# Kernel tuning notes

Measured on AMD Instinct MI355X. Metric: run time of the kernel, lower is better.

## Reference

```python
import jax, jax.numpy as jnp
import numpy as np

RES = 64; UP = 128; LATENT = 16; RGB_LAT = 15
XYZ_MIN = -1.0; XYZ_MAX = 1.0
STEPSIZE = 0.5; NEAR = 0.2; FAR = 6.0; BG = 1.0
VOXEL = (XYZ_MAX - XYZ_MIN) / RES
ALPHA_INIT = 1e-4
ACT_SHIFT = float(np.log(1.0 / (1.0 - ALPHA_INIT) - 1.0))
N_SAMPLES = int(np.linalg.norm(np.array([2 * RES + 1] * 3)) / STEPSIZE) + 1
BN_SCALE = (1.0 + 1e-5) ** -0.5  # eval-mode BatchNorm with running_mean=0, running_var=1
EPS = 1e-12
FREQS = [float(2.0 ** i) for i in range(6)]

def _sobel_kernel():
    hd = np.array([-1., -2., 0., 2., 1.]); h = np.array([1., 4., 6., 4., 1.])
    kx = np.einsum('i,j,k->ijk', hd, h, h)
    ky = np.einsum('i,j,k->ijk', h, hd, h)
    kz = np.einsum('i,j,k->ijk', h, h, hd)
    K = np.stack([kx, ky, kz])[:, None]
    return jnp.asarray(K / np.abs(K).max(), dtype=jnp.float32)

SOBEL_K = _sobel_kernel()

def _normalize(x, axis=-1):
    return x / jnp.maximum(jnp.linalg.norm(x, axis=axis, keepdims=True), EPS)

def _conv1x1(x, w, b):
    return jnp.einsum('oc,cdhw->odhw', w, x) + b[:, None, None, None]

def _bn(x, g, b):
    return x * (BN_SCALE * g)[:, None, None, None] + b[:, None, None, None]

def _prelu(x, a):
    return jnp.where(x >= 0, x, a[:, None, None, None] * x)

def _grid_reg(grid, c1_w, c1_b, bn1_g, bn1_b, pr1_a, c2_w, c2_b, bn2_g, bn2_b, pr2_a, c3_w, c3_b):
    x1 = _prelu(_bn(_conv1x1(grid, c1_w, c1_b), bn1_g, bn1_b), pr1_a)
    x2 = _prelu(_bn(_conv1x1(jnp.concatenate([x1, grid], 0), c2_w, c2_b), bn2_g, bn2_b), pr2_a)
    x3 = _conv1x1(jnp.concatenate([x1, x2, grid], 0), c3_w, c3_b)  # [(1+15)*8, R, R, R]
    # PixelShuffle3d(scale=2): [16*8,R,R,R] -> [16,2R,2R,2R]
    up = x3.reshape(LATENT, 2, 2, 2, RES, RES, RES).transpose(0, 4, 1, 5, 2, 6, 3).reshape(LATENT, UP, UP, UP)
    sob = jax.lax.conv_general_dilated(up[:1][None], SOBEL_K, (1, 1, 1), [(2, 2)] * 3,
                                       dimension_numbers=('NCDHW', 'OIDHW', 'NCDHW'))[0]
    normals = -_normalize(sob, axis=0)
    return up.transpose(1, 2, 3, 0), normals.transpose(1, 2, 3, 0)  # [UP,UP,UP,16], [UP,UP,UP,3]

def _trilinear(feat, p):
    # feat: [UP,UP,UP,C] indexed as world (x,y,z); p: [...,3] world coords. align_corners=True.
    u = jnp.clip((p - XYZ_MIN) / (XYZ_MAX - XYZ_MIN) * (UP - 1), 0.0, UP - 1.0)
    i0 = jnp.clip(jnp.floor(u).astype(jnp.int32), 0, UP - 2)
    f = u - i0.astype(u.dtype)
    ix, iy, iz = i0[..., 0], i0[..., 1], i0[..., 2]
    fx, fy, fz = f[..., 0:1], f[..., 1:2], f[..., 2:3]
    def g(dx, dy, dz):
        return feat[ix + dx, iy + dy, iz + dz]
    c00 = g(0, 0, 0) * (1 - fz) + g(0, 0, 1) * fz
    c01 = g(0, 1, 0) * (1 - fz) + g(0, 1, 1) * fz
    c10 = g(1, 0, 0) * (1 - fz) + g(1, 0, 1) * fz
    c11 = g(1, 1, 0) * (1 - fz) + g(1, 1, 1) * fz
    c0 = c00 * (1 - fy) + c01 * fy
    c1 = c10 * (1 - fy) + c11 * fy
    return c0 * (1 - fx) + c1 * fx

def _sample_ray(rays_o, rays_d):
    vec = jnp.where(rays_d == 0, 1e-6, rays_d)
    rate_a = (XYZ_MAX - rays_o) / vec
    rate_b = (XYZ_MIN - rays_o) / vec
    t_min = jnp.clip(jnp.minimum(rate_a, rate_b).max(-1), NEAR, FAR)
    t_max = jnp.clip(jnp.maximum(rate_a, rate_b).min(-1), NEAR, FAR)
    mask_ray = t_max <= t_min
    rng = jnp.arange(N_SAMPLES, dtype=rays_o.dtype)  # eval mode: no jitter
    step = STEPSIZE * VOXEL * rng
    interpx = t_min[:, None] + step[None] / jnp.linalg.norm(rays_d, axis=-1, keepdims=True)
    pts = rays_o[:, None, :] + rays_d[:, None, :] * interpx[..., None]
    outbox = mask_ray[:, None] | ((pts < XYZ_MIN) | (pts > XYZ_MAX)).any(-1)
    return pts, outbox

def _forward(rays_o, rays_d, viewdirs, grid, c1_w, c1_b, bn1_g, bn1_b, pr1_a, c2_w, c2_b, bn2_g, bn2_b, pr2_a, c3_w, c3_b, mlp_w0, mlp_b0, mlp_w1, mlp_b1, mlp_w2, mlp_b2, mlp_w3, mlp_b3):
    feat_grid, normals_grid = _grid_reg(grid, c1_w, c1_b, bn1_g, bn1_b, pr1_a, c2_w, c2_b, bn2_g, bn2_b, pr2_a, c3_w, c3_b)
    pts, outbox = _sample_ray(rays_o, rays_d)
    inside = ~outbox
    N, S = pts.shape[:2]
    pf = pts.reshape(-1, 3)

    def alpha_fn(p):
        d = _trilinear(feat_grid, p)[..., 0]
        return 1.0 - jnp.exp(-jax.nn.softplus(d + ACT_SHIFT) * STEPSIZE)

    alpha_flat, vjp_fn = jax.vjp(alpha_fn, pf)
    grads = vjp_fn(jnp.ones_like(alpha_flat))[0]  # d alpha / d point (analytic normals)
    nd = -_normalize(grads).reshape(N, S, 3)
    nd = jnp.where(inside[..., None], nd, 0.0)
    alpha = jnp.where(inside, alpha_flat.reshape(N, S), 0.0)

    feat = _trilinear(feat_grid, pf)
    rgb_latent = feat[:, 1:].reshape(N, S, RGB_LAT)

    ns = -_normalize(_trilinear(normals_grid, pf)).reshape(N, S, 3)  # sobel normals
    ns = jnp.where(inside[..., None], ns, 0.0)

    v = jnp.broadcast_to(viewdirs[:, None, :], nd.shape)
    dot = jnp.sum(-v * nd, -1, keepdims=True)
    refdirs = 2.0 * dot * nd + v
    emb = jnp.concatenate([refdirs] + [f(refdirs * fr) for fr in FREQS for f in (jnp.sin, jnp.cos)], -1)
    hfeat = jnp.concatenate([rgb_latent, emb], -1)  # [N,S,54]
    h = jax.nn.relu(hfeat @ mlp_w0 + mlp_b0)
    h = jax.nn.relu(h @ mlp_w1 + mlp_b1)
    h = jax.nn.relu(h @ mlp_w2 + mlp_b2)
    rgb = jax.nn.sigmoid(h @ mlp_w3 + mlp_b3)
    rgb = jnp.where(inside[..., None], rgb, 0.0)

    t = jnp.cumprod(jnp.clip(1.0 - alpha, 1e-10, None), -1)
    alphainv = jnp.concatenate([jnp.ones_like(t[..., :1]), t], -1)
    weights = alpha * alphainv[..., :-1]
    rgb_m = (weights[..., None] * rgb).sum(-2) + alphainv[..., -1:] * BG
    depth = jnp.linalg.norm(rays_o[:, None, :] - pts, axis=-1)
    depth_m = (weights * depth).sum(-1) + alphainv[..., -1] * FAR
    disp = 1.0 / depth_m
    acc = weights.sum(-1)
    nm = (weights[..., None] * nd).sum(-2)
    sm = (weights[..., None] * ns).sum(-2)
    return jnp.concatenate([rgb_m, depth_m[..., None], disp[..., None], acc[..., None], nm, sm], -1)  # [N,12]

def setup_inputs() -> dict:
    key = jax.random.key(0)
    ks = jax.random.split(key, 16)
    N = 1024
    cam = jnp.array([0.0, 0.0, -2.5], dtype=jnp.float32)
    rays_o = cam + 0.05 * jax.random.normal(ks[0], (N, 3), dtype=jnp.float32)
    tgt = jax.random.uniform(ks[1], (N, 3), minval=-0.5, maxval=0.5, dtype=jnp.float32)
    d = tgt - rays_o
    viewdirs = d / jnp.linalg.norm(d, axis=-1, keepdims=True)
    def w(k, shape, s=0.1):
        return s * jax.random.normal(k, shape, dtype=jnp.float32)
    return dict(
        rays_o=rays_o, rays_d=d, viewdirs=viewdirs,
        grid=w(ks[2], (16, 64, 64, 64)),
        c1_w=w(ks[3], (64, 16)), c1_b=w(ks[4], (64,), 0.01),
        bn1_g=jnp.ones(64, jnp.float32), bn1_b=jnp.zeros(64, jnp.float32), pr1_a=0.25 * jnp.ones(64, jnp.float32),
        c2_w=w(ks[5], (64, 80)), c2_b=w(ks[6], (64,), 0.01),
        bn2_g=jnp.ones(64, jnp.float32), bn2_b=jnp.zeros(64, jnp.float32), pr2_a=0.25 * jnp.ones(64, jnp.float32),
        c3_w=w(ks[7], (128, 144)), c3_b=w(ks[8], (128,), 0.01),
        mlp_w0=w(ks[9], (54, 64)), mlp_b0=jnp.zeros(64, jnp.float32),
        mlp_w1=w(ks[10], (64, 64)), mlp_b1=jnp.zeros(64, jnp.float32),
        mlp_w2=w(ks[11], (64, 64)), mlp_b2=jnp.zeros(64, jnp.float32),
        mlp_w3=w(ks[12], (64, 3)), mlp_b3=jnp.zeros(3, jnp.float32))

def reference(rays_o, rays_d, viewdirs, grid, c1_w, c1_b, bn1_g, bn1_b, pr1_a, c2_w, c2_b, bn2_g, bn2_b, pr2_a, c3_w, c3_b, mlp_w0, mlp_b0, mlp_w1, mlp_b1, mlp_w2, mlp_b2, mlp_w3, mlp_b3):
    return _forward(rays_o, rays_d, viewdirs, grid, c1_w, c1_b, bn1_g, bn1_b, pr1_a, c2_w, c2_b, bn2_g, bn2_b, pr2_a, c3_w, c3_b, mlp_w0, mlp_b0, mlp_w1, mlp_b1, mlp_w2, mlp_b2, mlp_w3, mlp_b3)
```

## Files before the change

### kernel.cpp

```cpp
#include <hip/hip_runtime.h>
#include <math.h>

#define S_SAMPLES 447
#define ACT_SHIFT -9.210240366971207f
#define BN_SCALE_C 0.9999950000374997f
#define STEP_VOX 0.015625f

__device__ __forceinline__ unsigned f2bf_u(float f) {
    unsigned u = __float_as_uint(f);
    return (u + 0x7fffu + ((u >> 16) & 1u)) >> 16;
}
__device__ __forceinline__ float bf2f(unsigned short u) {
    return __uint_as_float(((unsigned)u) << 16);
}
__device__ __forceinline__ float bf_lo(unsigned u) { return __uint_as_float(u << 16); }
__device__ __forceinline__ float bf_hi(unsigned u) { return __uint_as_float(u & 0xffff0000u); }

typedef __attribute__((ext_vector_type(8))) short bf16x8;
typedef __attribute__((ext_vector_type(4))) float f32x4;

__global__ __launch_bounds__(256) void prep_kernel(
    const float* __restrict__ w1, const float* __restrict__ w2,
    const float* __restrict__ w3, const float* __restrict__ b3,
    const float* __restrict__ mw0, const float* __restrict__ mw1,
    const float* __restrict__ mw2,
    unsigned short* __restrict__ w1b, unsigned short* __restrict__ w2b,
    unsigned short* __restrict__ w3b, float* __restrict__ b3p,
    unsigned short* __restrict__ m0t, unsigned short* __restrict__ m1t,
    unsigned short* __restrict__ m2t)
{
    const int gid = blockIdx.x * 256 + threadIdx.x;
    const int gs = gridDim.x * 256;
    for (int idx = gid; idx < 2048; idx += gs) {
        const int o = idx >> 5, k = idx & 31;
        w1b[idx] = (k < 16) ? (unsigned short)f2bf_u(w1[o * 16 + k]) : 0;
    }
    for (int idx = gid; idx < 6144; idx += gs) {
        const int o = idx / 96, k = idx % 96;
        w2b[idx] = (k < 80) ? (unsigned short)f2bf_u(w2[o * 80 + k]) : 0;
    }
    for (int idx = gid; idx < 20480; idx += gs) {
        const int n = idx / 160, k = idx % 160;
        const int s = n >> 4, l = n & 15;
        const int o = l * 8 + s;
        float val = 0.f;
        if (k < 64)       val = w3[o * 144 + k];
        else if (k < 80)  val = w3[o * 144 + 128 + (k - 64)];
        else if (k >= 96) val = w3[o * 144 + 64 + (k - 96)];
        w3b[idx] = (unsigned short)f2bf_u(val);
    }
    for (int idx = gid; idx < 128; idx += gs) {
        const int o = idx;
        b3p[(o & 7) * 16 + (o >> 3)] = b3[o];
    }
    for (int idx = gid; idx < 4096; idx += gs) {
        const int o = idx >> 6, k = idx & 63;
        m0t[o * 64 + k] = (k < 54) ? (unsigned short)f2bf_u(mw0[k * 64 + o]) : 0;
    }
    for (int idx = gid; idx < 4096; idx += gs) {
        const int o = idx >> 6, k = idx & 63;
        m1t[o * 64 + k] = (unsigned short)f2bf_u(mw1[k * 64 + o]);
    }
    for (int idx = gid; idx < 4096; idx += gs) {
        const int o = idx >> 6, k = idx & 63;
        m2t[o * 64 + k] = (unsigned short)f2bf_u(mw2[k * 64 + o]);
    }
}

__global__ __launch_bounds__(128) void conv_fused_kernel(
    const float* __restrict__ grid,
    const unsigned short* __restrict__ w1b, const float* __restrict__ b1,
    const float* __restrict__ g1, const float* __restrict__ bb1, const float* __restrict__ a1,
    const unsigned short* __restrict__ w2b, const float* __restrict__ b2,
    const float* __restrict__ g2, const float* __restrict__ bb2, const float* __restrict__ a2,
    const unsigned short* __restrict__ w3b, const float* __restrict__ b3p,
    unsigned short* __restrict__ featb, float* __restrict__ dens)
{
    __shared__ __align__(16) unsigned short AT[64 * 168];
    unsigned short* Ct = AT;
    float* densT = (float*)(AT + 64 * 136);
    const int t = threadIdx.x;
    const int v0 = blockIdx.x * 64;

    for (int idx = t; idx < 512; idx += 128) {
        const int v = idx >> 3, c = idx & 7;
        *(unsigned*)(AT + v * 168 + 80 + c * 2) = 0;
    }
    {
        const int vv = t & 63, half = t >> 6;
        for (int c = half; c < 16; c += 2) {
            const float gv = grid[(size_t)c * 262144 + v0 + vv];
            AT[vv * 168 + 64 + c] = (unsigned short)f2bf_u(gv);
        }
    }
    __syncthreads();

    const int wv = t >> 6, lane = t & 63;
    const int quad = lane >> 4, l16 = lane & 15;
    const int ch0 = 32 * wv + l16;

    {
        f32x4 acc[4][2];
        float gs[2], bb[2], al[2];
#pragma unroll
        for (int nt = 0; nt < 2; ++nt) {
            const int ch = ch0 + 16 * nt;
            const float bch = b1[ch];
            gs[nt] = BN_SCALE_C * g1[ch]; bb[nt] = bb1[ch]; al[nt] = a1[ch];
#pragma unroll
            for (int mt = 0; mt < 4; ++mt) {
                acc[mt][nt][0] = bch; acc[mt][nt][1] = bch;
                acc[mt][nt][2] = bch; acc[mt][nt][3] = bch;
            }
        }
        const int k0 = 8 * quad;
        bf16x8 a[4], b[2];
#pragma unroll
        for (int mt = 0; mt < 4; ++mt)
            a[mt] = __builtin_bit_cast(bf16x8, *(const uint4*)(AT + (16 * mt + l16) * 168 + 64 + k0));
#pragma unroll
        for (int nt = 0; nt < 2; ++nt)
            b[nt] = __builtin_bit_cast(bf16x8, *(const uint4*)(w1b + (ch0 + 16 * nt) * 32 + k0));
#pragma unroll
        for (int mt = 0; mt < 4; ++mt)
#pragma unroll
            for (int nt = 0; nt < 2; ++nt)
                acc[mt][nt] = __builtin_amdgcn_mfma_f32_16x16x32_bf16(a[mt], b[nt], acc[mt][nt], 0, 0, 0);
        __syncthreads();
#pragma unroll
        for (int mt = 0; mt < 4; ++mt)
#pragma unroll
            for (int nt = 0; nt < 2; ++nt)
#pragma unroll
                for (int reg = 0; reg < 4; ++reg) {
                    float x = acc[mt][nt][reg] * gs[nt] + bb[nt];
                    x = (x >= 0.f) ? x : al[nt] * x;
                    AT[(16 * mt + 4 * quad + reg) * 168 + ch0 + 16 * nt] = (unsigned short)f2bf_u(x);
                }
    }
    __syncthreads();

    {
        f32x4 acc[4][2];
        float gs[2], bb[2], al[2];
#pragma unroll
        for (int nt = 0; nt < 2; ++nt) {
            const int ch = ch0 + 16 * nt;
            const float bch = b2[ch];
            gs[nt] = BN_SCALE_C * g2[ch]; bb[nt] = bb2[ch]; al[nt] = a2[ch];
#pragma unroll
            for (int mt = 0; mt < 4; ++mt) {
                acc[mt][nt][0] = bch; acc[mt][nt][1] = bch;
                acc[mt][nt][2] = bch; acc[mt][nt][3] = bch;
            }
        }
#pragma unroll
        for (int kq = 0; kq < 3; ++kq) {
            const int k0 = 32 * kq + 8 * quad;
            bf16x8 a[4], b[2];
#pragma unroll
            for (int mt = 0; mt < 4; ++mt)
                a[mt] = __builtin_bit_cast(bf16x8, *(const uint4*)(AT + (16 * mt + l16) * 168 + k0));
#pragma unroll
            for (int nt = 0; nt < 2; ++nt)
                b[nt] = __builtin_bit_cast(bf16x8, *(const uint4*)(w2b + (ch0 + 16 * nt) * 96 + k0));
#pragma unroll
            for (int mt = 0; mt < 4; ++mt)
#pragma unroll
                for (int nt = 0; nt < 2; ++nt)
                    acc[mt][nt] = __builtin_amdgcn_mfma_f32_16x16x32_bf16(a[mt], b[nt], acc[mt][nt], 0, 0, 0);
        }
        __syncthreads();
#pragma unroll
        for (int mt = 0; mt < 4; ++mt)
#pragma unroll
            for (int nt = 0; nt < 2; ++nt)
#pragma unroll
                for (int reg = 0; reg < 4; ++reg) {
                    float x = acc[mt][nt][reg] * gs[nt] + bb[nt];
                    x = (x >= 0.f) ? x : al[nt] * x;
                    AT[(16 * mt + 4 * quad + reg) * 168 + 96 + ch0 + 16 * nt] = (unsigned short)f2bf_u(x);
                }
    }
    __syncthreads();

    {
        f32x4 acc[4][4];
#pragma unroll
        for (int nt = 0; nt < 4; ++nt) {
            const float bv = b3p[64 * wv + 16 * nt + l16];
#pragma unroll
            for (int mt = 0; mt < 4; ++mt) {
                acc[mt][nt][0] = bv; acc[mt][nt][1] = bv;
                acc[mt][nt][2] = bv; acc[mt][nt][3] = bv;
            }
        }
#pragma unroll
        for (int kq = 0; kq < 5; ++kq) {
            const int k0 = 32 * kq + 8 * quad;
            bf16x8 a[4], b[4];
#pragma unroll
            for (int mt = 0; mt < 4; ++mt)
                a[mt] = __builtin_bit_cast(bf16x8, *(const uint4*)(AT + (16 * mt + l16) * 168 + k0));
#pragma unroll
            for (int nt = 0; nt < 4; ++nt)
                b[nt] = __builtin_bit_cast(bf16x8, *(const uint4*)(w3b + (size_t)(64 * wv + 16 * nt + l16) * 160 + k0));
#pragma unroll
            for (int mt = 0; mt < 4; ++mt)
#pragma unroll
                for (int nt = 0; nt < 4; ++nt)
                    acc[mt][nt] = __builtin_amdgcn_mfma_f32_16x16x32_bf16(a[mt], b[nt], acc[mt][nt], 0, 0, 0);
        }

        __syncthreads();

        if (l16 == 0) {
#pragma unroll
            for (int mt = 0; mt < 4; ++mt)
#pragma unroll
                for (int nt = 0; nt < 4; ++nt) {
                    const int s = 4 * wv + nt;
#pragma unroll
                    for (int reg = 0; reg < 4; ++reg)
                        densT[(16 * mt + 4 * quad + reg) * 8 + s] = acc[mt][nt][reg];
                }
        }
#pragma unroll
        for (int mt = 0; mt < 4; ++mt)
#pragma unroll
            for (int nt = 0; nt < 4; ++nt)
#pragma unroll
                for (int reg = 0; reg < 4; ++reg)
                    Ct[(16 * mt + 4 * quad + reg) * 136 + 64 * wv + 16 * nt + l16] =
                        (unsigned short)f2bf_u(acc[mt][nt][reg]);
    }
    __syncthreads();

    const int v = t >> 1, half = t & 1;
    const int vg = v0 + v;
    const int Z = vg & 63, Y = (vg >> 6) & 63, X = vg >> 12;
#pragma unroll
    for (int si = 0; si < 4; ++si) {
        const int s = 4 * half + si;
        const int d2 = (s >> 2) & 1, h2 = (s >> 1) & 1, w2i = s & 1;
        const int ubase = ((2 * X + d2) * 128 + (2 * Y + h2)) * 128 + (2 * Z + w2i);
        const uint4 q0 = *(const uint4*)(Ct + v * 136 + 64 * half + 16 * si);
        const uint4 q1 = *(const uint4*)(Ct + v * 136 + 64 * half + 16 * si + 8);
        *(uint4*)(featb + (size_t)ubase * 16)     = q0;
        *(uint4*)(featb + (size_t)ubase * 16 + 8) = q1;
        dens[ubase] = densT[v * 8 + s];
    }
}

__global__ __launch_bounds__(256) void sobelZ_kernel(const float* __restrict__ dens,
                                                     float2* __restrict__ zbuf)
{
    const int v = blockIdx.x * 256 + threadIdx.x;
    const int z = v & 127;
    float d[5];
#pragma unroll
    for (int k = 0; k < 5; ++k) {
        const int zz = z + k - 2;
        d[k] = (zz >= 0 && zz < 128) ? dens[v + (k - 2)] : 0.f;
    }
    const float az = d[0] + 4.f * d[1] + 6.f * d[2] + 4.f * d[3] + d[4];
    const float bz = -d[0] - 2.f * d[1] + 2.f * d[3] + d[4];
    zbuf[v] = make_float2(az, bz);
}

__global__ __launch_bounds__(256) void sobelY_kernel(const float2* __restrict__ zbuf,
                                                     float4* __restrict__ cbuf)
{
    const int v = blockIdx.x * 256 + threadIdx.x;
    const int y = (v >> 7) & 127;
    float2 e[5];
#pragma unroll
    for (int j = 0; j < 5; ++j) {
        const int yy = y + j - 2;
        e[j] = (yy >= 0 && yy < 128) ? zbuf[v + (j - 2) * 128] : make_float2(0.f, 0.f);
    }
    const float c1 = e[0].x + 4.f * e[1].x + 6.f * e[2].x + 4.f * e[3].x + e[4].x;
    const float c2 = -e[0].x - 2.f * e[1].x + 2.f * e[3].x + e[4].x;
    const float c3 = e[0].y + 4.f * e[1].y + 6.f * e[2].y + 4.f * e[3].y + e[4].y;
    cbuf[v] = make_float4(c1, c2, c3, 0.f);
}

__global__ __launch_bounds__(256) void sobelX_kernel(const float4* __restrict__ cbuf,
                                                     float* __restrict__ normals)
{
    const int v = blockIdx.x * 256 + threadIdx.x;
    const int x = v >> 14;
    float4 q[5];
#pragma unroll
    for (int i = 0; i < 5; ++i) {
        const int xx = x + i - 2;
        q[i] = (xx >= 0 && xx < 128) ? cbuf[v + (i - 2) * 16384]
                                     : make_float4(0.f, 0.f, 0.f, 0.f);
    }
    float sx = -q[0].x - 2.f * q[1].x + 2.f * q[3].x + q[4].x;
    float sy = q[0].y + 4.f * q[1].y + 6.f * q[2].y + 4.f * q[3].y + q[4].y;
    float sz = q[0].z + 4.f * q[1].z + 6.f * q[2].z + 4.f * q[3].z + q[4].z;
    sx *= (1.f / 72.f); sy *= (1.f / 72.f); sz *= (1.f / 72.f);
    const float n = sqrtf(sx * sx + sy * sy + sz * sz);
    const float inv = 1.f / fmaxf(n, 1e-12f);
    normals[v * 3 + 0] = -sx * inv;
    normals[v * 3 + 1] = -sy * inv;
    normals[v * 3 + 2] = -sz * inv;
}

__device__ __forceinline__ void mfma_layer(unsigned short* A,
                                           const unsigned short* __restrict__ Wg,
                                           const float* __restrict__ bias,
                                           const int wv, const int lane)
{
    const int quad = lane >> 4, l16 = lane & 15;
    f32x4 acc[4][4];
#pragma unroll
    for (int nt = 0; nt < 4; ++nt) {
        const float bv = bias[16 * nt + l16];
#pragma unroll
        for (int mt = 0; mt < 4; ++mt) {
            acc[mt][nt][0] = bv; acc[mt][nt][1] = bv;
            acc[mt][nt][2] = bv; acc[mt][nt][3] = bv;
        }
    }
    bf16x8 a[2][4], b[2][4];
#pragma unroll
    for (int kq = 0; kq < 2; ++kq) {
        const int k0 = 32 * kq + 8 * quad;
#pragma unroll
        for (int mt = 0; mt < 4; ++mt)
            a[kq][mt] = __builtin_bit_cast(bf16x8, *(const uint4*)(A + (64 * wv + 16 * mt + l16) * 72 + k0));
#pragma unroll
        for (int nt = 0; nt < 4; ++nt)
            b[kq][nt] = __builtin_bit_cast(bf16x8, *(const uint4*)(Wg + (16 * nt + l16) * 64 + k0));
    }
#pragma unroll
    for (int kq = 0; kq < 2; ++kq)
#pragma unroll
        for (int mt = 0; mt < 4; ++mt)
#pragma unroll
            for (int nt = 0; nt < 4; ++nt)
                acc[mt][nt] = __builtin_amdgcn_mfma_f32_16x16x32_bf16(a[kq][mt], b[kq][nt], acc[mt][nt], 0, 0, 0);
#pragma unroll
    for (int mt = 0; mt < 4; ++mt)
#pragma unroll
        for (int nt = 0; nt < 4; ++nt)
#pragma unroll
            for (int reg = 0; reg < 4; ++reg) {
                const float v = fmaxf(acc[mt][nt][reg], 0.f);
                A[(64 * wv + 16 * mt + 4 * quad + reg) * 72 + 16 * nt + l16] =
                    (unsigned short)f2bf_u(v);
            }
}

__global__ __launch_bounds__(128) void sample_kernel(
    const float* __restrict__ ro, const float* __restrict__ rd, const float* __restrict__ vd,
    const unsigned short* __restrict__ featb, const float* __restrict__ dens,
    const float* __restrict__ normals,
    const unsigned short* __restrict__ m0t, const float* __restrict__ mb0,
    const unsigned short* __restrict__ m1t, const float* __restrict__ mb1,
    const unsigned short* __restrict__ m2t, const float* __restrict__ mb2,
    const float* __restrict__ mw3, const float* __restrict__ mb3,
    float* __restrict__ sbuf, const int total)
{
    __shared__ __align__(16) unsigned short act[128 * 72];

    const int t = threadIdx.x;
    const int s = blockIdx.x * 128 + t;
    const bool live = (s < total);
    bool actv = false;
    float alpha = 0.f, ndx = 0.f, ndy = 0.f, ndz = 0.f;
    float nsx = 0.f, nsy = 0.f, nsz = 0.f, depth = 0.f;
    float hf[64];
#pragma unroll
    for (int q = 0; q < 64; ++q) hf[q] = 0.f;

    if (live) {
        const int r = s / S_SAMPLES;
        const int j = s - r * S_SAMPLES;

        const float ox = ro[r * 3 + 0], oy = ro[r * 3 + 1], oz = ro[r * 3 + 2];
        const float dx = rd[r * 3 + 0], dy = rd[r * 3 + 1], dz = rd[r * 3 + 2];
        const float vx = vd[r * 3 + 0], vy = vd[r * 3 + 1], vz = vd[r * 3 + 2];

        const float vecx = (dx == 0.f) ? 1e-6f : dx;
        const float vecy = (dy == 0.f) ? 1e-6f : dy;
        const float vecz = (dz == 0.f) ? 1e-6f : dz;
        const float rax = (1.f - ox) / vecx, rbx = (-1.f - ox) / vecx;
        const float ray2 = (1.f - oy) / vecy, rby = (-1.f - oy) / vecy;
        const float raz = (1.f - oz) / vecz, rbz = (-1.f - oz) / vecz;
        float tmin = fmaxf(fmaxf(fminf(rax, rbx), fminf(ray2, rby)), fminf(raz, rbz));
        float tmax = fminf(fminf(fmaxf(rax, rbx), fmaxf(ray2, rby)), fmaxf(raz, rbz));
        tmin = fminf(fmaxf(tmin, 0.2f), 6.0f);
        tmax = fminf(fmaxf(tmax, 0.2f), 6.0f);
        const bool mask_ray = (tmax <= tmin);

        const float ndr = sqrtf(dx * dx + dy * dy + dz * dz);
        const float interpx = tmin + (STEP_VOX * (float)j) / ndr;
        const float px = ox + dx * interpx;
        const float py = oy + dy * interpx;
        const float pz = oz + dz * interpx;
        const bool outbox = mask_ray || (px < -1.f) || (px > 1.f) || (py < -1.f) ||
                            (py > 1.f) || (pz < -1.f) || (pz > 1.f);
        actv = !outbox;
        if (actv) {
            const float ux = fminf(fmaxf((px + 1.f) * 63.5f, 0.f), 127.f);
            const float uy = fminf(fmaxf((py + 1.f) * 63.5f, 0.f), 127.f);
            const float uz = fminf(fmaxf((pz + 1.f) * 63.5f, 0.f), 127.f);
            const int ix = min(max((int)floorf(ux), 0), 126);
            const int iy = min(max((int)floorf(uy), 0), 126);
            const int iz = min(max((int)floorf(uz), 0), 126);
            const float fx = ux - (float)ix, fy = uy - (float)iy, fz = uz - (float)iz;

            float lat[15];
#pragma unroll
            for (int q = 0; q < 15; ++q) lat[q] = 0.f;
            float na0 = 0.f, na1 = 0.f, na2 = 0.f;
            float c0v[8];
#pragma unroll
            for (int cn = 0; cn < 8; ++cn) {
                const int adx = cn >> 2, ady = (cn >> 1) & 1, adz = cn & 1;
                const int vox = ((ix + adx) * 128 + (iy + ady)) * 128 + (iz + adz);
                const float w = (adx ? fx : 1.f - fx) * (ady ? fy : 1.f - fy) * (adz ? fz : 1.f - fz);
                c0v[cn] = dens[vox];
                const uint4* cp = (const uint4*)(featb + (size_t)vox * 16);
                const uint4 q0 = cp[0], q1 = cp[1];
                lat[0]  = fmaf(w, bf_hi(q0.x), lat[0]);
                lat[1]  = fmaf(w, bf_lo(q0.y), lat[1]);
                lat[2]  = fmaf(w, bf_hi(q0.y), lat[2]);
                lat[3]  = fmaf(w, bf_lo(q0.z), lat[3]);
                lat[4]  = fmaf(w, bf_hi(q0.z), lat[4]);
                lat[5]  = fmaf(w, bf_lo(q0.w), lat[5]);
                lat[6]  = fmaf(w, bf_hi(q0.w), lat[6]);
                lat[7]  = fmaf(w, bf_lo(q1.x), lat[7]);
                lat[8]  = fmaf(w, bf_hi(q1.x), lat[8]);
                lat[9]  = fmaf(w, bf_lo(q1.y), lat[9]);
                lat[10] = fmaf(w, bf_hi(q1.y), lat[10]);
                lat[11] = fmaf(w, bf_lo(q1.z), lat[11]);
                lat[12] = fmaf(w, bf_hi(q1.z), lat[12]);
                lat[13] = fmaf(w, bf_lo(q1.w), lat[13]);
                lat[14] = fmaf(w, bf_hi(q1.w), lat[14]);
                const float* np_ = normals + (size_t)vox * 3;
                na0 = fmaf(w, np_[0], na0);
                na1 = fmaf(w, np_[1], na1);
                na2 = fmaf(w, np_[2], na2);
            }

            const float c00 = c0v[0] * (1.f - fz) + c0v[1] * fz;
            const float c01 = c0v[2] * (1.f - fz) + c0v[3] * fz;
            const float c10 = c0v[4] * (1.f - fz) + c0v[5] * fz;
            const float c11 = c0v[6] * (1.f - fz) + c0v[7] * fz;
            const float e0 = c00 * (1.f - fy) + c01 * fy;
            const float e1 = c10 * (1.f - fy) + c11 * fy;
            const float d0 = e0 * (1.f - fx) + e1 * fx;
            const float dfx = e1 - e0;
            const float dfy = (c01 - c00) * (1.f - fx) + (c11 - c10) * fx;
            const float dfz = ((c0v[1] - c0v[0]) * (1.f - fy) + (c0v[3] - c0v[2]) * fy) * (1.f - fx)
                            + ((c0v[5] - c0v[4]) * (1.f - fy) + (c0v[7] - c0v[6]) * fy) * fx;

            const float zin = d0 + ACT_SHIFT;
            const float splus = fmaxf(zin, 0.f) + log1pf(__expf(-fabsf(zin)));
            const float e = __expf(-splus * 0.5f);
            alpha = 1.f - e;
            const float sig = 1.f / (1.f + __expf(-zin));
            const float dad = e * 0.5f * sig;
            const float gx = dad * dfx * 63.5f;
            const float gy = dad * dfy * 63.5f;
            const float gz = dad * dfz * 63.5f;
            const float gn = sqrtf(gx * gx + gy * gy + gz * gz);
            const float gi = 1.f / fmaxf(gn, 1e-12f);
            ndx = -gx * gi; ndy = -gy * gi; ndz = -gz * gi;

            const float nn = sqrtf(na0 * na0 + na1 * na1 + na2 * na2);
            const float ni = 1.f / fmaxf(nn, 1e-12f);
            nsx = -na0 * ni; nsy = -na1 * ni; nsz = -na2 * ni;

            const float dotv = -(vx * ndx + vy * ndy + vz * ndz);
            const float rx = 2.f * dotv * ndx + vx;
            const float ry = 2.f * dotv * ndy + vy;
            const float rz = 2.f * dotv * ndz + vz;

#pragma unroll
            for (int q = 0; q < 15; ++q) hf[q] = lat[q];
            hf[15] = rx; hf[16] = ry; hf[17] = rz;
#pragma unroll
            for (int fi = 0; fi < 6; ++fi) {
                const float fr = (float)(1 << fi);
                hf[18 + fi * 6 + 0] = __sinf(rx * fr);
                hf[18 + fi * 6 + 1] = __sinf(ry * fr);
                hf[18 + fi * 6 + 2] = __sinf(rz * fr);
                hf[18 + fi * 6 + 3] = __cosf(rx * fr);
                hf[18 + fi * 6 + 4] = __cosf(ry * fr);
                hf[18 + fi * 6 + 5] = __cosf(rz * fr);
            }
            depth = interpx * ndr;
        }
    }

#pragma unroll
    for (int q = 0; q < 8; ++q) {
        uint4 st;
        st.x = f2bf_u(hf[8 * q + 0]) | (f2bf_u(hf[8 * q + 1]) << 16);
        st.y = f2bf_u(hf[8 * q + 2]) | (f2bf_u(hf[8 * q + 3]) << 16);
        st.z = f2bf_u(hf[8 * q + 4]) | (f2bf_u(hf[8 * q + 5]) << 16);
        st.w = f2bf_u(hf[8 * q + 6]) | (f2bf_u(hf[8 * q + 7]) << 16);
        *(uint4*)(act + t * 72 + 8 * q) = st;
    }
    __syncthreads();

    const int wv = t >> 6, lane = t & 63;
    mfma_layer(act, m0t, mb0, wv, lane);
    __syncthreads();
    mfma_layer(act, m1t, mb1, wv, lane);
    __syncthreads();
    mfma_layer(act, m2t, mb2, wv, lane);
    __syncthreads();

    if (live) {
        float* so = sbuf + (size_t)s * 12;
        if (actv) {
            float r0 = mb3[0], r1 = mb3[1], r2 = mb3[2];
            const unsigned short* hr = act + t * 72;
#pragma unroll
            for (int c8 = 0; c8 < 8; ++c8) {
                const uint4 hu = *(const uint4*)(hr + 8 * c8);
                const float h[8] = {bf_lo(hu.x), bf_hi(hu.x), bf_lo(hu.y), bf_hi(hu.y),
                                    bf_lo(hu.z), bf_hi(hu.z), bf_lo(hu.w), bf_hi(hu.w)};
#pragma unroll
                for (int u = 0; u < 8; ++u) {
                    const int c = 8 * c8 + u;
                    r0 = fmaf(h[u], mw3[c * 3 + 0], r0);
                    r1 = fmaf(h[u], mw3[c * 3 + 1], r1);
                    r2 = fmaf(h[u], mw3[c * 3 + 2], r2);
                }
            }
            so[0] = alpha;
            so[1] = 1.f / (1.f + __expf(-r0));
            so[2] = 1.f / (1.f + __expf(-r1));
            so[3] = 1.f / (1.f + __expf(-r2));
            so[4] = ndx; so[5] = ndy; so[6] = ndz;
            so[7] = nsx; so[8] = nsy; so[9] = nsz;
            so[10] = depth;
            so[11] = 0.f;
        } else {
#pragma unroll
            for (int q = 0; q < 12; ++q) so[q] = 0.f;
        }
    }
}

__global__ __launch_bounds__(64) void reduce_kernel(const float* __restrict__ sbuf,
                                                    float* __restrict__ out)
{
    const int r = blockIdx.x;
    const int lane = threadIdx.x;
    const int per = (S_SAMPLES + 63) / 64;
    const int j0 = lane * per;
    const int j1 = min(S_SAMPLES, j0 + per);

    float p = 1.f;
    for (int j = j0; j < j1; ++j) {
        const float a = sbuf[((size_t)r * S_SAMPLES + j) * 12];
        p *= fmaxf(1.f - a, 1e-10f);
    }
    float scan = p;
#pragma unroll
    for (int off = 1; off < 64; off <<= 1) {
        const float nv = __shfl_up(scan, (unsigned)off, 64);
        if (lane >= off) scan *= nv;
    }
    const float total = __shfl(scan, 63, 64);
    float pref = __shfl_up(scan, 1u, 64);
    if (lane == 0) pref = 1.f;

    float s0 = 0, s1 = 0, s2 = 0, s3 = 0, s4 = 0, s5 = 0, s6 = 0, s7 = 0, s8 = 0, s9 = 0, s10 = 0;
    for (int j = j0; j < j1; ++j) {
        const float* sp_ = sbuf + ((size_t)r * S_SAMPLES + j) * 12;
        const float a = sp_[0];
        const float w = a * pref;
        pref *= fmaxf(1.f - a, 1e-10f);
        s0 = fmaf(w, sp_[1], s0);
        s1 = fmaf(w, sp_[2], s1);
        s2 = fmaf(w, sp_[3], s2);
        s3 = fmaf(w, sp_[10], s3);
        s4 += w;
        s5 = fmaf(w, sp_[4], s5);
        s6 = fmaf(w, sp_[5], s6);
        s7 = fmaf(w, sp_[6], s7);
        s8 = fmaf(w, sp_[7], s8);
        s9 = fmaf(w, sp_[8], s9);
        s10 = fmaf(w, sp_[9], s10);
    }
#pragma unroll
    for (int m = 32; m >= 1; m >>= 1) {
        s0 += __shfl_xor(s0, m, 64);
        s1 += __shfl_xor(s1, m, 64);
        s2 += __shfl_xor(s2, m, 64);
        s3 += __shfl_xor(s3, m, 64);
        s4 += __shfl_xor(s4, m, 64);
        s5 += __shfl_xor(s5, m, 64);
        s6 += __shfl_xor(s6, m, 64);
        s7 += __shfl_xor(s7, m, 64);
        s8 += __shfl_xor(s8, m, 64);
        s9 += __shfl_xor(s9, m, 64);
        s10 += __shfl_xor(s10, m, 64);
    }
    if (lane == 0) {
        const float dm = s3 + total * 6.0f;
        out[r * 12 + 0] = s0 + total;
        out[r * 12 + 1] = s1 + total;
        out[r * 12 + 2] = s2 + total;
        out[r * 12 + 3] = dm;
        out[r * 12 + 4] = 1.f / dm;
        out[r * 12 + 5] = s4;
        out[r * 12 + 6] = s5; out[r * 12 + 7] = s6; out[r * 12 + 8] = s7;
        out[r * 12 + 9] = s8; out[r * 12 + 10] = s9; out[r * 12 + 11] = s10;
    }
}

extern "C" void kernel_launch(void* const* d_in, const int* in_sizes, int n_in,
                              void* d_out, int out_size, void* d_ws, size_t ws_size,
                              hipStream_t stream)
{
    (void)n_in; (void)out_size; (void)ws_size;
    const float* rays_o   = (const float*)d_in[0];
    const float* rays_d   = (const float*)d_in[1];
    const float* viewdirs = (const float*)d_in[2];
    const float* grid     = (const float*)d_in[3];
    const float* c1_w  = (const float*)d_in[4];
    const float* c1_b  = (const float*)d_in[5];
    const float* bn1_g = (const float*)d_in[6];
    const float* bn1_b = (const float*)d_in[7];
    const float* pr1_a = (const float*)d_in[8];
    const float* c2_w  = (const float*)d_in[9];
    const float* c2_b  = (const float*)d_in[10];
    const float* bn2_g = (const float*)d_in[11];
    const float* bn2_b = (const float*)d_in[12];
    const float* pr2_a = (const float*)d_in[13];
    const float* c3_w  = (const float*)d_in[14];
    const float* c3_b  = (const float*)d_in[15];
    const float* mw0 = (const float*)d_in[16];
    const float* mb0 = (const float*)d_in[17];
    const float* mw1 = (const float*)d_in[18];
    const float* mb1 = (const float*)d_in[19];
    const float* mw2 = (const float*)d_in[20];
    const float* mb2 = (const float*)d_in[21];
    const float* mw3 = (const float*)d_in[22];
    const float* mb3 = (const float*)d_in[23];

    const int N = in_sizes[0] / 3;
    const int total = N * S_SAMPLES;

    float* wsf = (float*)d_ws;
    unsigned short* featb = (unsigned short*)wsf;
    float* dens    = wsf + (size_t)16777216;
    float* normals = wsf + (size_t)18874368;
    float2* zbuf   = (float2*)(wsf + (size_t)25165824);
    float4* cbuf   = (float4*)(wsf + (size_t)29360128);
    float* sbuf    = wsf + (size_t)39845888;
    float* b3p = wsf + (size_t)45337600;
    unsigned short* w1b = (unsigned short*)(wsf + (size_t)45337728);
    unsigned short* w2b = (unsigned short*)(wsf + (size_t)45338752);
    unsigned short* w3b = (unsigned short*)(wsf + (size_t)45341824);
    unsigned short* m0t = (unsigned short*)(wsf + (size_t)45352064);
    unsigned short* m1t = (unsigned short*)(wsf + (size_t)45354112);
    unsigned short* m2t = (unsigned short*)(wsf + (size_t)45356160);

    prep_kernel<<<64, 256, 0, stream>>>(c1_w, c2_w, c3_w, c3_b, mw0, mw1, mw2,
                                        w1b, w2b, w3b, b3p, m0t, m1t, m2t);
    conv_fused_kernel<<<4096, 128, 0, stream>>>(grid, w1b, c1_b, bn1_g, bn1_b, pr1_a,
                                                w2b, c2_b, bn2_g, bn2_b, pr2_a,
                                                w3b, b3p, featb, dens);
    sobelZ_kernel<<<8192, 256, 0, stream>>>(dens, zbuf);
    sobelY_kernel<<<8192, 256, 0, stream>>>(zbuf, cbuf);
    sobelX_kernel<<<8192, 256, 0, stream>>>(cbuf, normals);
    const int sblocks = (total + 127) / 128;
    sample_kernel<<<sblocks, 128, 0, stream>>>(rays_o, rays_d, viewdirs, featb, dens, normals,
                                               m0t, mb0, m1t, mb1, m2t, mb2, mw3, mb3,
                                               sbuf, total);
    reduce_kernel<<<N, 64, 0, stream>>>(sbuf, (float*)d_out);
}
```

Baseline: 259.7 us.

## Shrink conv and sample kernels to single-wavefront blocks of 64 threads

Rewrites conv_fused_kernel so one 64-thread wavefront handles 32 voxels and all output channels per block, and sample_kernel so each block holds one wavefront of 64 samples. The aim is smaller blocks, less LDS per block and more resident blocks per CU, which should ease barrier coupling between waves. In exchange each wave re-reads all the weights itself, launches twice as many blocks, and keeps more accumulator registers live in the conv kernel. mfma_layer now places the barriers inside the function.

```diff
diff --git a/kernel.cpp b/kernel.cpp
--- a/kernel.cpp
+++ b/kernel.cpp
@@ -67,7 +67,7 @@
     }
 }
 
-__global__ __launch_bounds__(128) void conv_fused_kernel(
+__global__ __launch_bounds__(64) void conv_fused_kernel(
     const float* __restrict__ grid,
     const unsigned short* __restrict__ w1b, const float* __restrict__ b1,
     const float* __restrict__ g1, const float* __restrict__ bb1, const float* __restrict__ a1,
@@ -76,80 +76,77 @@
     const unsigned short* __restrict__ w3b, const float* __restrict__ b3p,
     unsigned short* __restrict__ featb, float* __restrict__ dens)
 {
-    __shared__ __align__(16) unsigned short AT[64 * 168];
+    __shared__ __align__(16) unsigned short AT[32 * 168];
+    __shared__ float densT[32 * 8];
     unsigned short* Ct = AT;
-    float* densT = (float*)(AT + 64 * 136);
     const int t = threadIdx.x;
-    const int v0 = blockIdx.x * 64;
-
-    for (int idx = t; idx < 512; idx += 128) {
+    const int v0 = blockIdx.x * 32;
+
+    for (int idx = t; idx < 256; idx += 64) {
         const int v = idx >> 3, c = idx & 7;
         *(unsigned*)(AT + v * 168 + 80 + c * 2) = 0;
     }
+#pragma unroll
+    for (int i = 0; i < 8; ++i) {
+        const int c = 2 * i + (t >> 5);
+        const float gv = grid[(size_t)c * 262144 + v0 + (t & 31)];
+        AT[(t & 31) * 168 + 64 + c] = (unsigned short)f2bf_u(gv);
+    }
+    __syncthreads();
+
+    const int quad = t >> 4, l16 = t & 15;
+
     {
-        const int vv = t & 63, half = t >> 6;
-        for (int c = half; c < 16; c += 2) {
-            const float gv = grid[(size_t)c * 262144 + v0 + vv];
-            AT[vv * 168 + 64 + c] = (unsigned short)f2bf_u(gv);
-        }
-    }
-    __syncthreads();
-
-    const int wv = t >> 6, lane = t & 63;
-    const int quad = lane >> 4, l16 = lane & 15;
-    const int ch0 = 32 * wv + l16;
-
-    {
-        f32x4 acc[4][2];
-        float gs[2], bb[2], al[2];
-#pragma unroll
-        for (int nt = 0; nt < 2; ++nt) {
-            const int ch = ch0 + 16 * nt;
+        f32x4 acc[2][4];
+        float gs[4], bb[4], al[4];
+#pragma unroll
+        for (int nt = 0; nt < 4; ++nt) {
+            const int ch = 16 * nt + l16;
             const float bch = b1[ch];
             gs[nt] = BN_SCALE_C * g1[ch]; bb[nt] = bb1[ch]; al[nt] = a1[ch];
 #pragma unroll
-            for (int mt = 0; mt < 4; ++mt) {
+            for (int mt = 0; mt < 2; ++mt) {
                 acc[mt][nt][0] = bch; acc[mt][nt][1] = bch;
                 acc[mt][nt][2] = bch; acc[mt][nt][3] = bch;
             }
         }
         const int k0 = 8 * quad;
-        bf16x8 a[4], b[2];
-#pragma unroll
-        for (int mt = 0; mt < 4; ++mt)
+        bf16x8 a[2], b[4];
+#pragma unroll
+        for (int mt = 0; mt < 2; ++mt)
             a[mt] = __builtin_bit_cast(bf16x8, *(const uint4*)(AT + (16 * mt + l16) * 168 + 64 + k0));
 #pragma unroll
-        for (int nt = 0; nt < 2; ++nt)
-            b[nt] = __builtin_bit_cast(bf16x8, *(const uint4*)(w1b + (ch0 + 16 * nt) * 32 + k0));
-#pragma unroll
-        for (int mt = 0; mt < 4; ++mt)
-#pragma unroll
-            for (int nt = 0; nt < 2; ++nt)
+        for (int nt = 0; nt < 4; ++nt)
+            b[nt] = __builtin_bit_cast(bf16x8, *(const uint4*)(w1b + (16 * nt + l16) * 32 + k0));
+#pragma unroll
+        for (int mt = 0; mt < 2; ++mt)
+#pragma unroll
+            for (int nt = 0; nt < 4; ++nt)
                 acc[mt][nt] = __builtin_amdgcn_mfma_f32_16x16x32_bf16(a[mt], b[nt], acc[mt][nt], 0, 0, 0);
         __syncthreads();
 #pragma unroll
-        for (int mt = 0; mt < 4; ++mt)
-#pragma unroll
-            for (int nt = 0; nt < 2; ++nt)
+        for (int mt = 0; mt < 2; ++mt)
+#pragma unroll
+            for (int nt = 0; nt < 4; ++nt)
 #pragma unroll
                 for (int reg = 0; reg < 4; ++reg) {
                     float x = acc[mt][nt][reg] * gs[nt] + bb[nt];
                     x = (x >= 0.f) ? x : al[nt] * x;
-                    AT[(16 * mt + 4 * quad + reg) * 168 + ch0 + 16 * nt] = (unsigned short)f2bf_u(x);
+                    AT[(16 * mt + 4 * quad + reg) * 168 + 16 * nt + l16] = (unsigned short)f2bf_u(x);
                 }
     }
     __syncthreads();
 
     {
-        f32x4 acc[4][2];
-        float gs[2], bb[2], al[2];
-#pragma unroll
-        for (int nt = 0; nt < 2; ++nt) {
-            const int ch = ch0 + 16 * nt;
+        f32x4 acc[2][4];
+        float gs[4], bb[4], al[4];
+#pragma unroll
+        for (int nt = 0; nt < 4; ++nt) {
+            const int ch = 16 * nt + l16;
             const float bch = b2[ch];
             gs[nt] = BN_SCALE_C * g2[ch]; bb[nt] = bb2[ch]; al[nt] = a2[ch];
 #pragma unroll
-            for (int mt = 0; mt < 4; ++mt) {
+            for (int mt = 0; mt < 2; ++mt) {
                 acc[mt][nt][0] = bch; acc[mt][nt][1] = bch;
                 acc[mt][nt][2] = bch; acc[mt][nt][3] = bch;
             }
@@ -157,40 +154,40 @@
 #pragma unroll
         for (int kq = 0; kq < 3; ++kq) {
             const int k0 = 32 * kq + 8 * quad;
-            bf16x8 a[4], b[2];
-#pragma unroll
-            for (int mt = 0; mt < 4; ++mt)
+            bf16x8 a[2], b[4];
+#pragma unroll
+            for (int mt = 0; mt < 2; ++mt)
                 a[mt] = __builtin_bit_cast(bf16x8, *(const uint4*)(AT + (16 * mt + l16) * 168 + k0));
 #pragma unroll
-            for (int nt = 0; nt < 2; ++nt)
-                b[nt] = __builtin_bit_cast(bf16x8, *(const uint4*)(w2b + (ch0 + 16 * nt) * 96 + k0));
-#pragma unroll
-            for (int mt = 0; mt < 4; ++mt)
-#pragma unroll
-                for (int nt = 0; nt < 2; ++nt)
+            for (int nt = 0; nt < 4; ++nt)
+                b[nt] = __builtin_bit_cast(bf16x8, *(const uint4*)(w2b + (16 * nt + l16) * 96 + k0));
+#pragma unroll
+            for (int mt = 0; mt < 2; ++mt)
+#pragma unroll
+                for (int nt = 0; nt < 4; ++nt)
                     acc[mt][nt] = __builtin_amdgcn_mfma_f32_16x16x32_bf16(a[mt], b[nt], acc[mt][nt], 0, 0, 0);
         }
         __syncthreads();
 #pragma unroll
-        for (int mt = 0; mt < 4; ++mt)
-#pragma unroll
-            for (int nt = 0; nt < 2; ++nt)
+        for (int mt = 0; mt < 2; ++mt)
+#pragma unroll
+            for (int nt = 0; nt < 4; ++nt)
 #pragma unroll
                 for (int reg = 0; reg < 4; ++reg) {
                     float x = acc[mt][nt][reg] * gs[nt] + bb[nt];
                     x = (x >= 0.f) ? x : al[nt] * x;
-                    AT[(16 * mt + 4 * quad + reg) * 168 + 96 + ch0 + 16 * nt] = (unsigned short)f2bf_u(x);
+                    AT[(16 * mt + 4 * quad + reg) * 168 + 96 + 16 * nt + l16] = (unsigned short)f2bf_u(x);
                 }
     }
     __syncthreads();
 
     {
-        f32x4 acc[4][4];
-#pragma unroll
-        for (int nt = 0; nt < 4; ++nt) {
-            const float bv = b3p[64 * wv + 16 * nt + l16];
-#pragma unroll
-            for (int mt = 0; mt < 4; ++mt) {
+        f32x4 acc[2][8];
+#pragma unroll
+        for (int nt = 0; nt < 8; ++nt) {
+            const float bv = b3p[16 * nt + l16];
+#pragma unroll
+            for (int mt = 0; mt < 2; ++mt) {
                 acc[mt][nt][0] = bv; acc[mt][nt][1] = bv;
                 acc[mt][nt][2] = bv; acc[mt][nt][3] = bv;
             }
@@ -198,17 +195,17 @@
 #pragma unroll
         for (int kq = 0; kq < 5; ++kq) {
             const int k0 = 32 * kq + 8 * quad;
-            bf16x8 a[4], b[4];
-#pragma unroll
-            for (int mt = 0; mt < 4; ++mt)
+            bf16x8 a[2], b[8];
+#pragma unroll
+            for (int mt = 0; mt < 2; ++mt)
                 a[mt] = __builtin_bit_cast(bf16x8, *(const uint4*)(AT + (16 * mt + l16) * 168 + k0));
 #pragma unroll
-            for (int nt = 0; nt < 4; ++nt)
-                b[nt] = __builtin_bit_cast(bf16x8, *(const uint4*)(w3b + (size_t)(64 * wv + 16 * nt + l16) * 160 + k0));
-#pragma unroll
-            for (int mt = 0; mt < 4; ++mt)
-#pragma unroll
-                for (int nt = 0; nt < 4; ++nt)
+            for (int nt = 0; nt < 8; ++nt)
+                b[nt] = __builtin_bit_cast(bf16x8, *(const uint4*)(w3b + (size_t)(16 * nt + l16) * 160 + k0));
+#pragma unroll
+            for (int mt = 0; mt < 2; ++mt)
+#pragma unroll
+                for (int nt = 0; nt < 8; ++nt)
                     acc[mt][nt] = __builtin_amdgcn_mfma_f32_16x16x32_bf16(a[mt], b[nt], acc[mt][nt], 0, 0, 0);
         }
 
@@ -216,22 +213,20 @@
 
         if (l16 == 0) {
 #pragma unroll
-            for (int mt = 0; mt < 4; ++mt)
-#pragma unroll
-                for (int nt = 0; nt < 4; ++nt) {
-                    const int s = 4 * wv + nt;
+            for (int mt = 0; mt < 2; ++mt)
+#pragma unroll
+                for (int nt = 0; nt < 8; ++nt)
 #pragma unroll
                     for (int reg = 0; reg < 4; ++reg)
-                        densT[(16 * mt + 4 * quad + reg) * 8 + s] = acc[mt][nt][reg];
-                }
-        }
-#pragma unroll
-        for (int mt = 0; mt < 4; ++mt)
-#pragma unroll
-            for (int nt = 0; nt < 4; ++nt)
+                        densT[(16 * mt + 4 * quad + reg) * 8 + nt] = acc[mt][nt][reg];
+        }
+#pragma unroll
+        for (int mt = 0; mt < 2; ++mt)
+#pragma unroll
+            for (int nt = 0; nt < 8; ++nt)
 #pragma unroll
                 for (int reg = 0; reg < 4; ++reg)
-                    Ct[(16 * mt + 4 * quad + reg) * 136 + 64 * wv + 16 * nt + l16] =
+                    Ct[(16 * mt + 4 * quad + reg) * 136 + 16 * nt + l16] =
                         (unsigned short)f2bf_u(acc[mt][nt][reg]);
     }
     __syncthreads();
@@ -244,8 +239,8 @@
         const int s = 4 * half + si;
         const int d2 = (s >> 2) & 1, h2 = (s >> 1) & 1, w2i = s & 1;
         const int ubase = ((2 * X + d2) * 128 + (2 * Y + h2)) * 128 + (2 * Z + w2i);
-        const uint4 q0 = *(const uint4*)(Ct + v * 136 + 64 * half + 16 * si);
-        const uint4 q1 = *(const uint4*)(Ct + v * 136 + 64 * half + 16 * si + 8);
+        const uint4 q0 = *(const uint4*)(Ct + v * 136 + 16 * s);
+        const uint4 q1 = *(const uint4*)(Ct + v * 136 + 16 * s + 8);
         *(uint4*)(featb + (size_t)ubase * 16)     = q0;
         *(uint4*)(featb + (size_t)ubase * 16 + 8) = q1;
         dens[ubase] = densT[v * 8 + s];
@@ -311,7 +306,7 @@
 __device__ __forceinline__ void mfma_layer(unsigned short* A,
                                            const unsigned short* __restrict__ Wg,
                                            const float* __restrict__ bias,
-                                           const int wv, const int lane)
+                                           const int lane)
 {
     const int quad = lane >> 4, l16 = lane & 15;
     f32x4 acc[4][4];
@@ -330,7 +325,7 @@
         const int k0 = 32 * kq + 8 * quad;
 #pragma unroll
         for (int mt = 0; mt < 4; ++mt)
-            a[kq][mt] = __builtin_bit_cast(bf16x8, *(const uint4*)(A + (64 * wv + 16 * mt + l16) * 72 + k0));
+            a[kq][mt] = __builtin_bit_cast(bf16x8, *(const uint4*)(A + (16 * mt + l16) * 72 + k0));
 #pragma unroll
         for (int nt = 0; nt < 4; ++nt)
             b[kq][nt] = __builtin_bit_cast(bf16x8, *(const uint4*)(Wg + (16 * nt + l16) * 64 + k0));
@@ -342,6 +337,7 @@
 #pragma unroll
             for (int nt = 0; nt < 4; ++nt)
                 acc[mt][nt] = __builtin_amdgcn_mfma_f32_16x16x32_bf16(a[kq][mt], b[kq][nt], acc[mt][nt], 0, 0, 0);
+    __syncthreads();
 #pragma unroll
     for (int mt = 0; mt < 4; ++mt)
 #pragma unroll
@@ -349,12 +345,13 @@
 #pragma unroll
             for (int reg = 0; reg < 4; ++reg) {
                 const float v = fmaxf(acc[mt][nt][reg], 0.f);
-                A[(64 * wv + 16 * mt + 4 * quad + reg) * 72 + 16 * nt + l16] =
+                A[(16 * mt + 4 * quad + reg) * 72 + 16 * nt + l16] =
                     (unsigned short)f2bf_u(v);
             }
-}
-
-__global__ __launch_bounds__(128) void sample_kernel(
+    __syncthreads();
+}
+
+__global__ __launch_bounds__(64) void sample_kernel(
     const float* __restrict__ ro, const float* __restrict__ rd, const float* __restrict__ vd,
     const unsigned short* __restrict__ featb, const float* __restrict__ dens,
     const float* __restrict__ normals,
@@ -364,10 +361,10 @@
     const float* __restrict__ mw3, const float* __restrict__ mb3,
     float* __restrict__ sbuf, const int total)
 {
-    __shared__ __align__(16) unsigned short act[128 * 72];
+    __shared__ __align__(16) unsigned short act[64 * 72];
 
     const int t = threadIdx.x;
-    const int s = blockIdx.x * 128 + t;
+    const int s = blockIdx.x * 64 + t;
     const bool live = (s < total);
     bool actv = false;
     float alpha = 0.f, ndx = 0.f, ndy = 0.f, ndz = 0.f;
@@ -509,13 +506,9 @@
     }
     __syncthreads();
 
-    const int wv = t >> 6, lane = t & 63;
-    mfma_layer(act, m0t, mb0, wv, lane);
-    __syncthreads();
-    mfma_layer(act, m1t, mb1, wv, lane);
-    __syncthreads();
-    mfma_layer(act, m2t, mb2, wv, lane);
-    __syncthreads();
+    mfma_layer(act, m0t, mb0, t);
+    mfma_layer(act, m1t, mb1, t);
+    mfma_layer(act, m2t, mb2, t);
 
     if (live) {
         float* so = sbuf + (size_t)s * 12;
@@ -669,15 +662,15 @@
 
     prep_kernel<<<64, 256, 0, stream>>>(c1_w, c2_w, c3_w, c3_b, mw0, mw1, mw2,
                                         w1b, w2b, w3b, b3p, m0t, m1t, m2t);
-    conv_fused_kernel<<<4096, 128, 0, stream>>>(grid, w1b, c1_b, bn1_g, bn1_b, pr1_a,
-                                                w2b, c2_b, bn2_g, bn2_b, pr2_a,
-                                                w3b, b3p, featb, dens);
+    conv_fused_kernel<<<8192, 64, 0, stream>>>(grid, w1b, c1_b, bn1_g, bn1_b, pr1_a,
+                                               w2b, c2_b, bn2_g, bn2_b, pr2_a,
+                                               w3b, b3p, featb, dens);
     sobelZ_kernel<<<8192, 256, 0, stream>>>(dens, zbuf);
     sobelY_kernel<<<8192, 256, 0, stream>>>(zbuf, cbuf);
     sobelX_kernel<<<8192, 256, 0, stream>>>(cbuf, normals);
-    const int sblocks = (total + 127) / 128;
-    sample_kernel<<<sblocks, 128, 0, stream>>>(rays_o, rays_d, viewdirs, featb, dens, normals,
-                                               m0t, mb0, m1t, mb1, m2t, mb2, mw3, mb3,
-                                               sbuf, total);
+    const int sblocks = (total + 63) / 64;
+    sample_kernel<<<sblocks, 64, 0, stream>>>(rays_o, rays_d, viewdirs, featb, dens, normals,
+                                              m0t, mb0, m1t, mb1, m2t, mb2, mw3, mb3,
+                                              sbuf, total);
     reduce_kernel<<<N, 64, 0, stream>>>(sbuf, (float*)d_out);
 }
```

After: 242.9 us. 1.07x faster.
